# Kernel optimization log

Hardware: AMD Instinct MI355X
Metric: run time of the kernel (lower is better)

## Reference

```python
import jax, jax.numpy as jnp
import numpy as np

B, P, C = 8, 16384, 5          # images, proposals/img, classes (incl. background)
K = 100                         # detections_per_img (greedy-NMS iterations)
SCORE_THRESH = 0.05
NMS_THRESH = 0.5
W_XY, W_WH = 10.0, 5.0          # bbox_reg_weights (10,10,5,5)
BBOX_XFORM_CLIP = float(np.log(1000.0 / 16.0))
NEG = jnp.float32(-1e30)


def setup_inputs() -> dict:
    key = jax.random.key(0)
    ks = jax.random.split(key, 8)
    N = B * P
    class_logits = jax.random.normal(ks[0], (N, C), jnp.float32)
    box_regression = jax.random.normal(ks[1], (N, C * 4), jnp.float32) * 0.1
    handside_logits = jax.random.normal(ks[2], (N, C), jnp.float32)
    dxdymag_logits = jax.random.normal(ks[3], (N, C * 3), jnp.float32)
    contact_logits = jax.random.normal(ks[4], (N, C * 5), jnp.float32)
    # valid proposal boxes x1<x2, y1<y2 inside an ~800x1216 image
    x1 = jax.random.uniform(ks[5], (B, P), jnp.float32) * 1100.0
    y1 = jax.random.uniform(ks[6], (B, P), jnp.float32) * 700.0
    wh = jax.random.uniform(ks[7], (B, P, 2), jnp.float32) * 100.0 + 4.0
    proposals = jnp.stack([x1, y1, x1 + wh[..., 0], y1 + wh[..., 1]], axis=-1)
    image_hw = jnp.array([800, 1216], jnp.int32)
    return dict(class_logits=class_logits, box_regression=box_regression,
                handside_logits=handside_logits, dxdymag_logits=dxdymag_logits,
                contact_logits=contact_logits, proposals=proposals, image_hw=image_hw)


def _decode(rel, props):
    # rel [N,C,4], props [N,4] -> [N,C,4] (torchvision BoxCoder.decode)
    w = props[:, 2] - props[:, 0]
    h = props[:, 3] - props[:, 1]
    cx = props[:, 0] + 0.5 * w
    cy = props[:, 1] + 0.5 * h
    dx = rel[..., 0] / W_XY
    dy = rel[..., 1] / W_XY
    dw = jnp.minimum(rel[..., 2] / W_WH, BBOX_XFORM_CLIP)
    dh = jnp.minimum(rel[..., 3] / W_WH, BBOX_XFORM_CLIP)
    pcx = dx * w[:, None] + cx[:, None]
    pcy = dy * h[:, None] + cy[:, None]
    pw = jnp.exp(dw) * w[:, None]
    ph = jnp.exp(dh) * h[:, None]
    return jnp.stack([pcx - 0.5 * pw, pcy - 0.5 * ph,
                      pcx + 0.5 * pw, pcy + 0.5 * ph], axis=-1)


def _iou_one_vs_all(box, boxes):
    lt = jnp.maximum(box[:2], boxes[:, :2])
    rb = jnp.minimum(box[2:], boxes[:, 2:])
    whd = jnp.clip(rb - lt, 0.0)
    inter = whd[:, 0] * whd[:, 1]
    a1 = (box[2] - box[0]) * (box[3] - box[1])
    a2 = (boxes[:, 2] - boxes[:, 0]) * (boxes[:, 3] - boxes[:, 1])
    return inter / (a1 + a2 - inter)


def _nms_image(boxes, scores, labels):
    # class-aware greedy NMS (batched_nms coordinate-offset trick), fixed K iters.
    off = labels.astype(boxes.dtype) * (jax.lax.stop_gradient(boxes).max() + 1.0)
    obox = jax.lax.stop_gradient(boxes) + off[:, None]

    def step(s, _):
        i = jnp.argmax(s)
        keep = s[i] > NEG * 0.5
        iou = _iou_one_vs_all(obox[i], obox)
        s = jnp.where((iou > NMS_THRESH) & keep, NEG, s)
        s = s.at[i].set(NEG)
        return s, (i, keep)

    _, (idx, keep) = jax.lax.scan(step, scores, None, length=K)
    return idx, keep


def reference(class_logits, box_regression, handside_logits, dxdymag_logits,
              contact_logits, proposals, image_hw):
    N = class_logits.shape[0]
    pred_boxes = _decode(box_regression.reshape(N, C, 4), proposals.reshape(-1, 4))
    pred_scores = jax.nn.softmax(class_logits, axis=-1)          # [N,C]
    pred_sides = (jax.nn.sigmoid(handside_logits) > 0.5).astype(jnp.float32)
    pred_dxdy = dxdymag_logits.reshape(N, C, 3)
    pred_contacts = jnp.argmax(contact_logits.reshape(N, C, 5), axis=2)
    # clip boxes to image (image_shape = (H, W))
    Hh = image_hw[0].astype(jnp.float32)
    Ww = image_hw[1].astype(jnp.float32)
    xs = jnp.clip(pred_boxes[..., 0::2], 0.0, Ww)
    ys = jnp.clip(pred_boxes[..., 1::2], 0.0, Hh)
    pred_boxes = jnp.stack([xs[..., 0], ys[..., 0], xs[..., 1], ys[..., 1]], -1)
    # drop background class, flatten per image (class-fastest order, as torch reshape)
    Cm1 = C - 1
    boxes = pred_boxes[:, 1:].reshape(B, P * Cm1, 4)
    scores = pred_scores[:, 1:].reshape(B, P * Cm1)
    sides = pred_sides[:, 1:].reshape(B, P * Cm1)
    dxdy = pred_dxdy[:, 1:].reshape(B, P * Cm1, 3)
    contacts = pred_contacts[:, 1:].reshape(B, P * Cm1)
    labels = jnp.broadcast_to(jnp.tile(jnp.arange(1, C), P), (B, P * Cm1))
    # score thresholding via masking (scores <= thresh never selected)
    ms = jnp.where(scores > SCORE_THRESH, scores, NEG)
    idx, keep = jax.vmap(_nms_image)(boxes, ms, labels)          # [B,K]
    kf = keep.astype(jnp.float32)
    out_boxes = jnp.take_along_axis(boxes, idx[:, :, None], 1) * kf[:, :, None]
    out_scores = jnp.take_along_axis(scores, idx, 1) * kf
    out_labels = jnp.where(keep, jnp.take_along_axis(labels, idx, 1), 0)
    out_sides = jnp.take_along_axis(sides, idx, 1) * kf
    out_dxdy = jnp.take_along_axis(dxdy, idx[:, :, None], 1) * kf[:, :, None]
    out_contacts = jnp.where(keep, jnp.take_along_axis(contacts, idx, 1), 0)
    return (out_boxes, out_scores, out_labels, out_sides, out_dxdy, out_contacts, keep)
```

## Files before the change

### kernel.cpp

```cpp
#include <hip/hip_runtime.h>
#include <cstdint>

typedef unsigned int u32;
typedef unsigned long long u64;

constexpr int B_ = 8;
constexpr int P_ = 16384;
constexpr int K_ = 100;
constexpr int M_ = P_ * 4;
constexpr int TSEL = 192;
constexpr int CAP = 256;
constexpr u32 BASE13 = 0x3D4CCCCEu >> 13;
constexpr int NBP = 4608;
constexpr float SCORE_T = 0.05f;
constexpr float CLIPV = 4.135166556742356f;

__device__ inline int aphys(int i) {
  return (i < CAP) ? ((((i & 63) + ((i >> 6) << 2)) & 63) | (i & 192)) : i;
}

__global__ __launch_bounds__(256) void prep_kernel(
    const float* __restrict__ logits,
    const float* __restrict__ boxreg,
    const float* __restrict__ props,
    const int*  __restrict__ image_hw,
    float* __restrict__ wboxes,
    float* __restrict__ wscores,
    float* __restrict__ wblockmax)
{
  const int n = blockIdx.x * 256 + threadIdx.x;

  float l[5];
#pragma unroll
  for (int i = 0; i < 5; ++i) l[i] = logits[n * 5 + i];
  float mx = l[0];
#pragma unroll
  for (int i = 1; i < 5; ++i) mx = fmaxf(mx, l[i]);
  float e[5]; float ssum = 0.f;
#pragma unroll
  for (int i = 0; i < 5; ++i) { e[i] = expf(l[i] - mx); ssum += e[i]; }

  const float4 pr = reinterpret_cast<const float4*>(props)[n];
  const float w  = pr.z - pr.x;
  const float h  = pr.w - pr.y;
  const float cx = pr.x + 0.5f * w;
  const float cy = pr.y + 0.5f * h;
  const float Hf = (float)image_hw[0];
  const float Wf = (float)image_hw[1];

  float bmax = 0.f;
  float sc[4];
#pragma unroll
  for (int c = 1; c < 5; ++c) {
    const float4 rel = reinterpret_cast<const float4*>(boxreg)[n * 5 + c];
    const float dx = rel.x / 10.0f;
    const float dy = rel.y / 10.0f;
    const float dw = fminf(rel.z / 5.0f, CLIPV);
    const float dh = fminf(rel.w / 5.0f, CLIPV);
    const float pcx = dx * w + cx;
    const float pcy = dy * h + cy;
    const float pw = expf(dw) * w;
    const float ph = expf(dh) * h;
    float x1 = pcx - 0.5f * pw, y1 = pcy - 0.5f * ph;
    float x2 = pcx + 0.5f * pw, y2 = pcy + 0.5f * ph;
    x1 = fminf(fmaxf(x1, 0.f), Wf);
    x2 = fminf(fmaxf(x2, 0.f), Wf);
    y1 = fminf(fmaxf(y1, 0.f), Hf);
    y2 = fminf(fmaxf(y2, 0.f), Hf);
    reinterpret_cast<float4*>(wboxes)[n * 4 + (c - 1)] = make_float4(x1, y1, x2, y2);
    bmax = fmaxf(bmax, fmaxf(fmaxf(x1, x2), fmaxf(y1, y2)));
    sc[c - 1] = e[c] / ssum;
  }
  reinterpret_cast<float4*>(wscores)[n] = make_float4(sc[0], sc[1], sc[2], sc[3]);

  __shared__ float red[256];
  red[threadIdx.x] = bmax;
  __syncthreads();
#pragma unroll
  for (int off = 128; off > 0; off >>= 1) {
    if (threadIdx.x < off) red[threadIdx.x] = fmaxf(red[threadIdx.x], red[threadIdx.x + off]);
    __syncthreads();
  }
  if (threadIdx.x == 0) wblockmax[blockIdx.x] = red[0];
}

__global__ __launch_bounds__(1024) void nms_kernel(
    const float* __restrict__ wboxes, const float* __restrict__ wscores,
    const float* __restrict__ wblockmax,
    const float* __restrict__ handside, const float* __restrict__ dxdymag,
    const float* __restrict__ contact, float* __restrict__ out)
{
  const int b = blockIdx.x, t = threadIdx.x;
  const float4* boxes4 = reinterpret_cast<const float4*>(wboxes);
  const float4* sc4 = reinterpret_cast<const float4*>(wscores) + (size_t)b * (M_ / 4);

  __shared__ u32   hist[NBP];
  __shared__ int   wavesum[16];
  __shared__ float maxv_s;
  __shared__ u32   X_s;
  __shared__ int   cnt_s;
  __shared__ u64   kall[CAP];
  __shared__ u64   skey[CAP];
  __shared__ float4 cb4[CAP + K_];
  __shared__ float carea[CAP + K_];
  __shared__ float cscf[CAP + K_];
  __shared__ int   cj[CAP + K_];
  __shared__ u64   supmask[CAP * 4];
  __shared__ u64   km[4];
  __shared__ int   chg;
  __shared__ int   kidx[K_];
  __shared__ int   kcount_s, nslow_s;
  __shared__ u64   red2[1024];
  __shared__ u64   bitmap[1024];

  if (t < 64) {
    float v = wblockmax[b * 64 + t];
#pragma unroll
    for (int off = 32; off > 0; off >>= 1) v = fmaxf(v, __shfl_xor(v, off));
    if (t == 0) maxv_s = v;
  }
  if (t == 0) { kcount_s = 0; nslow_s = 0; cnt_s = 0; X_s = BASE13 << 13; }
  for (int i = t; i < NBP; i += 1024) hist[i] = 0;
  __syncthreads();
  const float maxv1 = maxv_s + 1.0f;

  for (int i = t; i < M_ / 4; i += 1024) {
    const float4 v = sc4[i];
    const float ss[4] = {v.x, v.y, v.z, v.w};
#pragma unroll
    for (int c = 0; c < 4; ++c) {
      if (ss[c] > SCORE_T) {
        u32 bin = (__float_as_uint(ss[c]) >> 13) - BASE13;
        if (bin >= (u32)NBP) bin = NBP - 1;
        atomicAdd(&hist[bin], 1u);
      }
    }
  }
  __syncthreads();

  u32 hb[8]; int mysum = 0, inc = 0;
  const int lo = NBP - t * 8 - 8;
  if (t < 576) {
#pragma unroll
    for (int q = 0; q < 8; ++q) { hb[q] = hist[lo + q]; mysum += (int)hb[q]; }
    inc = mysum;
#pragma unroll
    for (int off = 1; off < 64; off <<= 1) {
      const int vv = __shfl_up(inc, off);
      if ((t & 63) >= off) inc += vv;
    }
    if ((t & 63) == 63) wavesum[t >> 6] = inc;
  }
  __syncthreads();
  if (t < 576) {
    int above = 0;
    for (int w = 0; w < (t >> 6); ++w) above += wavesum[w];
    inc += above;
    const int pre = inc - mysum;
    if (pre < TSEL && inc >= TSEL) {
      int cum = pre, kb = lo, qs = 7;
      for (int q = 7; q >= 0; --q) {
        cum += (int)hb[q];
        if (cum >= TSEL) { kb = lo + q; qs = q; break; }
      }
      u32 Xbin = (cum > CAP) ? (u32)(kb + 1)
                             : (u32)kb;
      X_s = (BASE13 + Xbin) << 13;
    }
  }
  if (t < CAP) kall[t] = 0ull;
  __syncthreads();
  const u32 X = X_s;

  for (int i = t; i < M_ / 4; i += 1024) {
    const float4 v = sc4[i];
    const float ss[4] = {v.x, v.y, v.z, v.w};
    const int j0 = i * 4;
#pragma unroll
    for (int c = 0; c < 4; ++c) {
      if (ss[c] > SCORE_T) {
        const u32 bb = __float_as_uint(ss[c]);
        if (bb >= X) {
          const int pos = atomicAdd(&cnt_s, 1);
          if (pos < CAP) kall[pos] = ((u64)bb << 16) | (u64)(65535 - (j0 + c));
        }
      }
    }
  }
  __syncthreads();
  const int C = min(cnt_s, CAP);

  if (t < CAP) {
    const u64 my = kall[t];
    u32 r = 0;
    for (int u = 0; u < CAP; ++u) r += (kall[u] > my) ? 1u : 0u;
    if (t < C) skey[r] = my;
  }
  __syncthreads();

  if (t < C) {
    const u64 key = skey[t];
    const int j = 65535 - (int)(key & 0xFFFFull);
    const int cls = (j & 3) + 1;
    const float4 bx = boxes4[(size_t)b * M_ + j];
    const float offv = (float)cls * maxv1;
    const float ox1 = bx.x + offv, oy1 = bx.y + offv;
    const float ox2 = bx.z + offv, oy2 = bx.w + offv;
    const int ph = aphys(t);
    cb4[ph] = make_float4(ox1, oy1, ox2, oy2);
    carea[ph] = (ox2 - ox1) * (oy2 - oy1);
    cscf[ph] = __uint_as_float((u32)(key >> 16));
    cj[ph] = j;
  }
  __syncthreads();

  for (int task = t; task < C * 4; task += 1024) {
    const int i = task >> 2, wq = task & 3;
    const float4 ib = cb4[aphys(i)];
    const float ia = carea[aphys(i)];
    u64 m = 0;
    const int qb = wq * 64, qe = min(qb + 64, C);
    for (int q = qb; q < qe; ++q) {
      if (q == i) continue;
      const int qp = aphys(q);
      const float4 qbx = cb4[qp];
      const float ltx = fmaxf(ib.x, qbx.x);
      const float lty = fmaxf(ib.y, qbx.y);
      const float rbx = fminf(ib.z, qbx.z);
      const float rby = fminf(ib.w, qbx.w);
      const float iw = fmaxf(rbx - ltx, 0.f);
      const float ih = fmaxf(rby - lty, 0.f);
      const float inter = iw * ih;
      const float iou = inter / (ia + carea[qp] - inter);
      if (iou > 0.5f) m |= 1ull << (q - qb);
    }
    supmask[i * 4 + wq] = m;
  }
  __syncthreads();

  const int wi = t >> 6, bi = t & 63;
  const u64 lowmask = bi ? (~0ull >> (64 - bi)) : 0ull;
  u64 rb0 = 0, rb1 = 0, rb2 = 0, rb3 = 0;
  const bool alive = (t < C);
  if (t < CAP) {
    rb0 = supmask[t * 4 + 0];
    rb1 = supmask[t * 4 + 1];
    rb2 = supmask[t * 4 + 2];
    rb3 = supmask[t * 4 + 3];
    const u64 m0 = (wi > 0) ? ~0ull : lowmask;
    const u64 m1 = (wi > 1) ? ~0ull : ((wi == 1) ? lowmask : 0ull);
    const u64 m2 = (wi > 2) ? ~0ull : ((wi == 2) ? lowmask : 0ull);
    const u64 m3 = (wi == 3) ? lowmask : 0ull;
    rb0 &= m0; rb1 &= m1; rb2 &= m2; rb3 &= m3;
    const u64 bal = __ballot(alive ? 1 : 0);
    if (bi == 0) km[wi] = bal;
  }
  __syncthreads();
  while (true) {
    if (t == 0) chg = 0;
    __syncthreads();
    u64 nb = 0;
    if (t < CAP) {
      const u64 k0 = km[0], k1 = km[1], k2 = km[2], k3 = km[3];
      const bool sup = ((rb0 & k0) | (rb1 & k1) | (rb2 & k2) | (rb3 & k3)) != 0ull;
      const bool kn = alive && !sup;
      nb = __ballot(kn ? 1 : 0);
      if (bi == 0 && nb != km[wi]) chg = 1;
    }
    __syncthreads();
    if (t < CAP && bi == 0) km[wi] = nb;
    __syncthreads();
    if (!chg) break;
  }

  if (t < CAP) {
    const u64 kw = km[wi];
    if ((kw >> bi) & 1ull) {
      int pb = 0;
      if (wi > 0) pb += __popcll(km[0]);
      if (wi > 1) pb += __popcll(km[1]);
      if (wi > 2) pb += __popcll(km[2]);
      pb += __popcll(kw & lowmask);
      if (pb < K_) kidx[pb] = t;
    }
    if (t == 0) {
      kcount_s = min(__popcll(km[0]) + __popcll(km[1]) +
                     __popcll(km[2]) + __popcll(km[3]), K_);
    }
  }
  __syncthreads();

  if (kcount_s < K_) {
    bitmap[t] = 0ull;
    __syncthreads();
    while (true) {
      u64 best = 0ull;
      for (int i = t; i < M_ / 4; i += 1024) {
        const float4 v = sc4[i];
        const float ss[4] = {v.x, v.y, v.z, v.w};
#pragma unroll
        for (int c = 0; c < 4; ++c) {
          if (ss[c] > SCORE_T) {
            const u32 bb = __float_as_uint(ss[c]);
            if (bb < X) {
              const int j = i * 4 + c;
              if (!((bitmap[j >> 6] >> (j & 63)) & 1ull)) {
                const u64 key = ((u64)bb << 16) | (u64)(65535 - j);
                if (key > best) best = key;
              }
            }
          }
        }
      }
      red2[t] = best;
      __syncthreads();
      for (int off = 512; off > 0; off >>= 1) {
        if (t < off && red2[t + off] > red2[t]) red2[t] = red2[t + off];
        __syncthreads();
      }
      const u64 wkey = red2[0];
      if (wkey == 0ull) break;
      if (t == 0) {
        const int j = 65535 - (int)(wkey & 0xFFFFull);
        bitmap[j >> 6] |= 1ull << (j & 63);
        const int cls = (j & 3) + 1;
        const float4 bx = boxes4[(size_t)b * M_ + j];
        const float offv = (float)cls * maxv1;
        const float ox1 = bx.x + offv, oy1 = bx.y + offv;
        const float ox2 = bx.z + offv, oy2 = bx.w + offv;
        const float ar = (ox2 - ox1) * (oy2 - oy1);
        bool sup = false;
        for (int k2 = 0; k2 < kcount_s; ++k2) {
          const int ki = aphys(kidx[k2]);
          const float4 kb = cb4[ki];
          const float ltx = fmaxf(kb.x, ox1);
          const float lty = fmaxf(kb.y, oy1);
          const float rbx = fminf(kb.z, ox2);
          const float rby = fminf(kb.w, oy2);
          const float iw = fmaxf(rbx - ltx, 0.f);
          const float ih = fmaxf(rby - lty, 0.f);
          const float inter = iw * ih;
          const float iou = inter / (carea[ki] + ar - inter);
          if (iou > 0.5f) { sup = true; break; }
        }
        if (!sup) {
          const int slot = CAP + nslow_s;
          cb4[slot] = make_float4(ox1, oy1, ox2, oy2);
          carea[slot] = ar;
          cscf[slot] = __uint_as_float((u32)(wkey >> 16));
          cj[slot] = j;
          kidx[kcount_s] = slot;
          ++nslow_s;
          ++kcount_s;
        }
      }
      __syncthreads();
      if (kcount_s >= K_) break;
    }
    __syncthreads();
  }
  __syncthreads();

  const int kc = kcount_s;
  if (t < K_) {
    const int r = t;
    float ob0 = 0.f, ob1 = 0.f, ob2 = 0.f, ob3 = 0.f;
    float osc = 0.f, olab = 0.f, oside = 0.f;
    float od0 = 0.f, od1 = 0.f, od2 = 0.f;
    float ocon = 0.f, okeep = 0.f;
    if (r < kc) {
      const int idx = kidx[r];
      const int ph = aphys(idx);
      const int j = cj[ph];
      const int cls = (j & 3) + 1;
      const int n = b * P_ + (j >> 2);
      const float4 bx = boxes4[(size_t)b * M_ + j];
      ob0 = bx.x; ob1 = bx.y; ob2 = bx.z; ob3 = bx.w;
      osc = cscf[ph];
      olab = (float)cls;
      oside = (handside[n * 5 + cls] > 0.f) ? 1.f : 0.f;
      od0 = dxdymag[n * 15 + cls * 3 + 0];
      od1 = dxdymag[n * 15 + cls * 3 + 1];
      od2 = dxdymag[n * 15 + cls * 3 + 2];
      float bvv = contact[n * 25 + cls * 5 + 0];
      int best = 0;
#pragma unroll
      for (int i = 1; i < 5; ++i) {
        const float ci = contact[n * 25 + cls * 5 + i];
        if (ci > bvv) { bvv = ci; best = i; }
      }
      ocon = (float)best;
      okeep = 1.f;
    }
    const int gb = b * K_ + r;
    out[gb * 4 + 0] = ob0;
    out[gb * 4 + 1] = ob1;
    out[gb * 4 + 2] = ob2;
    out[gb * 4 + 3] = ob3;
    out[3200 + gb] = osc;
    out[4000 + gb] = olab;
    out[4800 + gb] = oside;
    out[5600 + gb * 3 + 0] = od0;
    out[5600 + gb * 3 + 1] = od1;
    out[5600 + gb * 3 + 2] = od2;
    out[8000 + gb] = ocon;
    out[8800 + gb] = okeep;
  }
}

extern "C" void kernel_launch(void* const* d_in, const int* in_sizes, int n_in,
                              void* d_out, int out_size, void* d_ws, size_t ws_size,
                              hipStream_t stream) {
  const float* class_logits = (const float*)d_in[0];
  const float* box_reg      = (const float*)d_in[1];
  const float* handside     = (const float*)d_in[2];
  const float* dxdymag      = (const float*)d_in[3];
  const float* contact      = (const float*)d_in[4];
  const float* proposals    = (const float*)d_in[5];
  const int*   image_hw     = (const int*)d_in[6];
  float* out = (float*)d_out;

  char* ws = (char*)d_ws;
  float* wboxes    = (float*)ws;
  float* wscores   = (float*)(ws + (size_t)8 * 1024 * 1024);
  float* wblockmax = (float*)(ws + (size_t)10 * 1024 * 1024);

  prep_kernel<<<dim3(512), dim3(256), 0, stream>>>(
      class_logits, box_reg, proposals, image_hw, wboxes, wscores, wblockmax);
  nms_kernel<<<dim3(B_), dim3(1024), 0, stream>>>(
      wboxes, wscores, wblockmax, handside, dxdymag, contact, out);
}
```

Measured before the change: 51.82 us.

## Split histogram, threshold, and compaction out of per-image NMS block into grid-wide kernels

The score histogram now builds inside the prep kernel with global atomics. A small per-image kernel finds the selection threshold, and a grid-wide compaction kernel gathers candidate keys. This replaces two serial 64K-element scans that ran inside a single 1024-thread block per image, which used only 8 blocks. The NMS kernel shrinks to 512 threads and skips the slow fallback scan when no candidates remain below the threshold. The cost is extra launches, a memset, and contended global atomics on the histogram and counters.

```diff
diff --git a/kernel.cpp b/kernel.cpp
--- a/kernel.cpp
+++ b/kernel.cpp
@@ -10,8 +10,8 @@
 constexpr int M_ = P_ * 4;
 constexpr int TSEL = 192;
 constexpr int CAP = 256;
+constexpr int NBP = 4608;
 constexpr u32 BASE13 = 0x3D4CCCCEu >> 13;
-constexpr int NBP = 4608;
 constexpr float SCORE_T = 0.05f;
 constexpr float CLIPV = 4.135166556742356f;
 
@@ -26,9 +26,11 @@
     const int*  __restrict__ image_hw,
     float* __restrict__ wboxes,
     float* __restrict__ wscores,
-    float* __restrict__ wblockmax)
+    float* __restrict__ wblockmax,
+    u32*   __restrict__ hist)
 {
   const int n = blockIdx.x * 256 + threadIdx.x;
+  const int b = n >> 14;
 
   float l[5];
 #pragma unroll
@@ -69,7 +71,13 @@
     y2 = fminf(fmaxf(y2, 0.f), Hf);
     reinterpret_cast<float4*>(wboxes)[n * 4 + (c - 1)] = make_float4(x1, y1, x2, y2);
     bmax = fmaxf(bmax, fmaxf(fmaxf(x1, x2), fmaxf(y1, y2)));
-    sc[c - 1] = e[c] / ssum;
+    const float sv = e[c] / ssum;
+    sc[c - 1] = sv;
+    if (sv > SCORE_T) {
+      u32 bin = (__float_as_uint(sv) >> 13) - BASE13;
+      if (bin >= (u32)NBP) bin = NBP - 1;
+      atomicAdd(&hist[b * NBP + bin], 1u);
+    }
   }
   reinterpret_cast<float4*>(wscores)[n] = make_float4(sc[0], sc[1], sc[2], sc[3]);
 
@@ -84,21 +92,87 @@
   if (threadIdx.x == 0) wblockmax[blockIdx.x] = red[0];
 }
 
-__global__ __launch_bounds__(1024) void nms_kernel(
+__global__ __launch_bounds__(512) void thresh_kernel(
+    const u32* __restrict__ hist, u32* __restrict__ Xthr, int* __restrict__ remv)
+{
+  const int b = blockIdx.x, t = threadIdx.x;
+  const u32* h = hist + b * NBP;
+  const int lo = NBP - t * 9 - 9;
+  u32 hb[9]; int mysum = 0;
+#pragma unroll
+  for (int q = 0; q < 9; ++q) { hb[q] = h[lo + q]; mysum += (int)hb[q]; }
+
+  int inc = mysum;
+#pragma unroll
+  for (int off = 1; off < 64; off <<= 1) {
+    const int v = __shfl_up(inc, off);
+    if ((t & 63) >= off) inc += v;
+  }
+  __shared__ int wavesum[8];
+  __shared__ int tot_s;
+  if ((t & 63) == 63) wavesum[t >> 6] = inc;
+  __syncthreads();
+  int above = 0;
+  for (int w2 = 0; w2 < (t >> 6); ++w2) above += wavesum[w2];
+  inc += above;
+  if (t == 511) tot_s = inc;
+  __syncthreads();
+  const int tot = tot_s;
+  const int pre = inc - mysum;
+
+  if (tot < TSEL) {
+    if (t == 511) { Xthr[b] = BASE13 << 13; remv[b] = 0; }
+  } else if (pre < TSEL && inc >= TSEL) {
+    int cum = pre, kb = lo, qsel = 8;
+    for (int q = 8; q >= 0; --q) {
+      cum += (int)hb[q];
+      if (cum >= TSEL) { kb = lo + q; qsel = q; break; }
+    }
+    int C = cum;
+    u32 Xbin;
+    if (C > CAP) { C -= (int)hb[qsel]; Xbin = (u32)(kb + 1); }
+    else Xbin = (u32)kb;
+    Xthr[b] = (BASE13 + Xbin) << 13;
+    remv[b] = tot - C;
+  }
+}
+
+__global__ __launch_bounds__(256) void compact_kernel(
+    const float* __restrict__ wscores, const u32* __restrict__ Xthr,
+    int* __restrict__ selcnt, u64* __restrict__ keybuf)
+{
+  const int n = blockIdx.x * 256 + threadIdx.x;
+  const int b = n >> 14;
+  const u32 X = Xthr[b];
+  const float4 v = reinterpret_cast<const float4*>(wscores)[n];
+  const float ss[4] = {v.x, v.y, v.z, v.w};
+  const int j0 = (n & (P_ - 1)) * 4;
+#pragma unroll
+  for (int c = 0; c < 4; ++c) {
+    if (ss[c] > SCORE_T) {
+      const u32 bb = __float_as_uint(ss[c]);
+      if (bb >= X) {
+        const int pos = atomicAdd(&selcnt[b], 1);
+        if (pos < CAP) keybuf[b * CAP + pos] = ((u64)bb << 16) | (u64)(65535 - (j0 + c));
+      }
+    }
+  }
+}
+
+__global__ __launch_bounds__(512) void nms_kernel(
     const float* __restrict__ wboxes, const float* __restrict__ wscores,
-    const float* __restrict__ wblockmax,
+    const float* __restrict__ wblockmax, const u32* __restrict__ Xthr,
+    const int* __restrict__ remv, const int* __restrict__ selcnt,
+    const u64* __restrict__ keybuf,
     const float* __restrict__ handside, const float* __restrict__ dxdymag,
     const float* __restrict__ contact, float* __restrict__ out)
 {
   const int b = blockIdx.x, t = threadIdx.x;
   const float4* boxes4 = reinterpret_cast<const float4*>(wboxes);
   const float4* sc4 = reinterpret_cast<const float4*>(wscores) + (size_t)b * (M_ / 4);
-
-  __shared__ u32   hist[NBP];
-  __shared__ int   wavesum[16];
+  const u32 X = Xthr[b];
+
   __shared__ float maxv_s;
-  __shared__ u32   X_s;
-  __shared__ int   cnt_s;
   __shared__ u64   kall[CAP];
   __shared__ u64   skey[CAP];
   __shared__ float4 cb4[CAP + K_];
@@ -110,7 +184,7 @@
   __shared__ int   chg;
   __shared__ int   kidx[K_];
   __shared__ int   kcount_s, nslow_s;
-  __shared__ u64   red2[1024];
+  __shared__ u64   red2[512];
   __shared__ u64   bitmap[1024];
 
   if (t < 64) {
@@ -119,76 +193,11 @@
     for (int off = 32; off > 0; off >>= 1) v = fmaxf(v, __shfl_xor(v, off));
     if (t == 0) maxv_s = v;
   }
-  if (t == 0) { kcount_s = 0; nslow_s = 0; cnt_s = 0; X_s = BASE13 << 13; }
-  for (int i = t; i < NBP; i += 1024) hist[i] = 0;
+  if (t == 0) { kcount_s = 0; nslow_s = 0; }
+  const int C = min(selcnt[b], CAP);
+  if (t < CAP) kall[t] = (t < C) ? keybuf[b * CAP + t] : 0ull;
   __syncthreads();
   const float maxv1 = maxv_s + 1.0f;
-
-  for (int i = t; i < M_ / 4; i += 1024) {
-    const float4 v = sc4[i];
-    const float ss[4] = {v.x, v.y, v.z, v.w};
-#pragma unroll
-    for (int c = 0; c < 4; ++c) {
-      if (ss[c] > SCORE_T) {
-        u32 bin = (__float_as_uint(ss[c]) >> 13) - BASE13;
-        if (bin >= (u32)NBP) bin = NBP - 1;
-        atomicAdd(&hist[bin], 1u);
-      }
-    }
-  }
-  __syncthreads();
-
-  u32 hb[8]; int mysum = 0, inc = 0;
-  const int lo = NBP - t * 8 - 8;
-  if (t < 576) {
-#pragma unroll
-    for (int q = 0; q < 8; ++q) { hb[q] = hist[lo + q]; mysum += (int)hb[q]; }
-    inc = mysum;
-#pragma unroll
-    for (int off = 1; off < 64; off <<= 1) {
-      const int vv = __shfl_up(inc, off);
-      if ((t & 63) >= off) inc += vv;
-    }
-    if ((t & 63) == 63) wavesum[t >> 6] = inc;
-  }
-  __syncthreads();
-  if (t < 576) {
-    int above = 0;
-    for (int w = 0; w < (t >> 6); ++w) above += wavesum[w];
-    inc += above;
-    const int pre = inc - mysum;
-    if (pre < TSEL && inc >= TSEL) {
-      int cum = pre, kb = lo, qs = 7;
-      for (int q = 7; q >= 0; --q) {
-        cum += (int)hb[q];
-        if (cum >= TSEL) { kb = lo + q; qs = q; break; }
-      }
-      u32 Xbin = (cum > CAP) ? (u32)(kb + 1)
-                             : (u32)kb;
-      X_s = (BASE13 + Xbin) << 13;
-    }
-  }
-  if (t < CAP) kall[t] = 0ull;
-  __syncthreads();
-  const u32 X = X_s;
-
-  for (int i = t; i < M_ / 4; i += 1024) {
-    const float4 v = sc4[i];
-    const float ss[4] = {v.x, v.y, v.z, v.w};
-    const int j0 = i * 4;
-#pragma unroll
-    for (int c = 0; c < 4; ++c) {
-      if (ss[c] > SCORE_T) {
-        const u32 bb = __float_as_uint(ss[c]);
-        if (bb >= X) {
-          const int pos = atomicAdd(&cnt_s, 1);
-          if (pos < CAP) kall[pos] = ((u64)bb << 16) | (u64)(65535 - (j0 + c));
-        }
-      }
-    }
-  }
-  __syncthreads();
-  const int C = min(cnt_s, CAP);
 
   if (t < CAP) {
     const u64 my = kall[t];
@@ -214,7 +223,7 @@
   }
   __syncthreads();
 
-  for (int task = t; task < C * 4; task += 1024) {
+  for (int task = t; task < C * 4; task += 512) {
     const int i = task >> 2, wq = task & 3;
     const float4 ib = cb4[aphys(i)];
     const float ia = carea[aphys(i)];
@@ -290,12 +299,12 @@
   }
   __syncthreads();
 
-  if (kcount_s < K_) {
-    bitmap[t] = 0ull;
+  if (kcount_s < K_ && remv[b] > 0) {
+    for (int i = t; i < 1024; i += 512) bitmap[i] = 0ull;
     __syncthreads();
     while (true) {
       u64 best = 0ull;
-      for (int i = t; i < M_ / 4; i += 1024) {
+      for (int i = t; i < M_ / 4; i += 512) {
         const float4 v = sc4[i];
         const float ss[4] = {v.x, v.y, v.z, v.w};
 #pragma unroll
@@ -314,7 +323,7 @@
       }
       red2[t] = best;
       __syncthreads();
-      for (int off = 512; off > 0; off >>= 1) {
+      for (int off = 256; off > 0; off >>= 1) {
         if (t < off && red2[t + off] > red2[t]) red2[t] = red2[t + off];
         __syncthreads();
       }
@@ -421,12 +430,21 @@
   float* out = (float*)d_out;
 
   char* ws = (char*)d_ws;
-  float* wboxes    = (float*)ws;
-  float* wscores   = (float*)(ws + (size_t)8 * 1024 * 1024);
-  float* wblockmax = (float*)(ws + (size_t)10 * 1024 * 1024);
-
+  u32*   hist      = (u32*)  ws;
+  int*   selcnt    = (int*)  (ws + 147456);
+  u32*   Xthr      = (u32*)  (ws + 147488);
+  int*   remv      = (int*)  (ws + 147520);
+  float* wblockmax = (float*)(ws + 147584);
+  u64*   keybuf    = (u64*)  (ws + 149632);
+  float* wscores   = (float*)(ws + 262144);
+  float* wboxes    = (float*)(ws + 2359296);
+
+  hipMemsetAsync(ws, 0, 147488, stream);
   prep_kernel<<<dim3(512), dim3(256), 0, stream>>>(
-      class_logits, box_reg, proposals, image_hw, wboxes, wscores, wblockmax);
-  nms_kernel<<<dim3(B_), dim3(1024), 0, stream>>>(
-      wboxes, wscores, wblockmax, handside, dxdymag, contact, out);
-}
+      class_logits, box_reg, proposals, image_hw, wboxes, wscores, wblockmax, hist);
+  thresh_kernel<<<dim3(B_), dim3(512), 0, stream>>>(hist, Xthr, remv);
+  compact_kernel<<<dim3(512), dim3(256), 0, stream>>>(wscores, Xthr, selcnt, keybuf);
+  nms_kernel<<<dim3(B_), dim3(512), 0, stream>>>(
+      wboxes, wscores, wblockmax, Xthr, remv, selcnt, keybuf,
+      handside, dxdymag, contact, out);
+}
```

Result: slower. 87.08 us (+68.0%).
